# Optimization experiments

Hardware: AMD Instinct MI355X
Metric: run time of the kernel (lower is better)

The kernel has to match this reference:

```python
import jax, jax.numpy as jnp
import numpy as np

B, T, N = 16, 2048, 64
NUM_RATES, GRAPH_H, GCN_H, GATE_H, RATE_E = 8, 32, 32, 64, 16
F = T // 2 + 1


def _directional_fill(values, observed):
    # values: [B,T,N] float, observed: [B,T,N] bool. Sequential carry-forward fill.
    def step(carry, inp):
        last, has = carry
        v, obs = inp
        last = jnp.where(obs, v, last)
        has = has | obs
        filled = jnp.where(obs, v, jnp.where(has, last, jnp.zeros_like(last)))
        return (last, has), (filled, has)

    b, t, n = values.shape
    init = (jnp.zeros((b, n), values.dtype), jnp.zeros((b, n), dtype=bool))
    _, (filled, avail) = jax.lax.scan(step, init, (values.swapaxes(0, 1), observed.swapaxes(0, 1)))
    return filled.swapaxes(0, 1), avail.swapaxes(0, 1)


def warm_start_fill(values, missing_mask):
    observed = ~missing_mask.astype(bool)
    seed = jnp.where(observed, values, jnp.zeros_like(values))
    f_fill, f_av = _directional_fill(values, observed)
    b_fill, b_av = _directional_fill(values[:, ::-1], observed[:, ::-1])
    b_fill, b_av = b_fill[:, ::-1], b_av[:, ::-1]
    missing = missing_mask.astype(bool)
    both = missing & f_av & b_av
    fonly = missing & f_av & ~b_av
    bonly = missing & ~f_av & b_av
    seed = jnp.where(both, 0.5 * (f_fill + b_fill), seed)
    seed = jnp.where(fonly, f_fill, seed)
    seed = jnp.where(bonly, b_fill, seed)
    return seed


def setup_inputs() -> dict:
    key = jax.random.key(0)
    ks = jax.random.split(key, 16)
    x_input = jax.random.normal(ks[0], (B, T, N), dtype=jnp.float32)
    model_missing_mask = (jax.random.uniform(ks[1], (B, T, N)) < 0.5).astype(jnp.float32)
    rate_id = jax.random.randint(ks[2], (N,), 0, NUM_RATES)
    s = lambda k, shape, d: jax.random.normal(k, shape, dtype=jnp.float32) * (1.0 / np.sqrt(d))
    return {
        "x_input": x_input,
        "model_missing_mask": model_missing_mask,
        "rate_id": rate_id,
        "node_emb": s(ks[3], (N, GRAPH_H), GRAPH_H),
        "gcn_w1": s(ks[4], (GCN_H,), 1),
        "gcn_b1": jnp.zeros((GCN_H,), jnp.float32),
        "gcn_w2": s(ks[5], (GCN_H,), GCN_H),
        "gcn_b2": jnp.zeros((), jnp.float32),
        "freq_re": s(ks[6], (F, N), 1),
        "freq_im": s(ks[7], (F, N), 1),
        "rate_table": s(ks[8], (NUM_RATES, RATE_E), 1),
        "gw1": s(ks[9], (6 + RATE_E, GATE_H), 6 + RATE_E),
        "gb1": jnp.zeros((GATE_H,), jnp.float32),
        "gw2": s(ks[10], (GATE_H, GATE_H), GATE_H),
        "gb2": jnp.zeros((GATE_H,), jnp.float32),
        "gw3": s(ks[11], (GATE_H, 2), GATE_H),
        "gb3": jnp.zeros((2,), jnp.float32),
    }


def _forward(x_input, model_missing_mask, rate_id, node_emb, gcn_w1, gcn_b1,
             gcn_w2, gcn_b2, freq_re, freq_im, rate_table, gw1, gb1, gw2, gb2, gw3, gb3):
    x_seed = warm_start_fill(x_input, model_missing_mask)

    # --- GCN expert: learned adjacency from node embeddings, 1-hop propagation ---
    scores = jax.nn.relu(node_emb @ node_emb.T)            # [N,N]
    adjacency = jax.nn.softmax(scores, axis=-1)            # [N,N]
    h = jax.nn.gelu(x_seed[..., None] * gcn_w1 + gcn_b1)   # [B,T,N,H]
    h = jnp.einsum('nm,btmh->btnh', adjacency, h)          # message passing
    x_gcn = jnp.einsum('btnh,h->btn', h, gcn_w2) + gcn_b2  # [B,T,N]

    # --- Frequency expert: learned complex filter in rfft space ---
    X = jnp.fft.rfft(x_seed, axis=1)                       # [B,F,N]
    filt = freq_re + 1j * freq_im                          # [F,N]
    x_freq = jnp.fft.irfft(X * filt, n=T, axis=1).astype(x_seed.dtype)

    # --- Gate ---
    rate_embed = jnp.broadcast_to(rate_table[rate_id][None, None], (B, T, N, RATE_E))
    feats = jnp.stack([x_seed, model_missing_mask, x_gcn, x_freq,
                       x_gcn - x_seed, x_freq - x_seed], axis=-1)  # [B,T,N,6]
    gate_in = jnp.concatenate([feats, rate_embed], axis=-1)        # [B,T,N,22]
    g = jax.nn.gelu(gate_in @ gw1 + gb1)
    g = jax.nn.gelu(g @ gw2 + gb2)
    logits = g @ gw3 + gb3                                          # [B,T,N,2]
    logits = logits - jnp.max(logits, axis=-1, keepdims=True)
    gate_weights = jax.nn.softmax(logits, axis=-1)

    experts = jnp.stack([x_gcn, x_freq], axis=-1)                   # [B,T,N,2]
    x_imputed = jnp.sum(gate_weights * experts, axis=-1)
    x_complete = jnp.where(model_missing_mask.astype(bool), x_imputed, x_input)
    return x_seed, x_gcn, x_freq, x_imputed, x_complete, gate_weights, adjacency


def reference(x_input, model_missing_mask, rate_id, node_emb, gcn_w1, gcn_b1,
              gcn_w2, gcn_b2, freq_re, freq_im, rate_table, gw1, gb1, gw2, gb2, gw3, gb3):
    return _forward(x_input, model_missing_mask, rate_id, node_emb, gcn_w1, gcn_b1,
                    gcn_w2, gcn_b2, freq_re, freq_im, rate_table, gw1, gb1, gw2, gb2, gw3, gb3)
```

## Files before the change

### kernel.cpp

```cpp
#include <hip/hip_runtime.h>
#include <cstdint>

#define S_ELEMS 2097152ull
#define TT 2048
#define NN 64

typedef __attribute__((ext_vector_type(8))) short bf16x8;
typedef __attribute__((ext_vector_type(4))) float f32x4;

__device__ __forceinline__ float gelu_f(float x) {
  float x2 = x * x;
  float z = -1.5957691216057308f * x * (1.0f + 0.044715f * x2);
  return __fdividef(x, 1.0f + __expf(z));
}

__device__ __forceinline__ float2 cmul(float2 a, float2 b) {
  return make_float2(a.x * b.x - a.y * b.y, a.x * b.y + a.y * b.x);
}

__device__ __forceinline__ uint16_t f2bf(float x) {
  uint32_t u = __float_as_uint(x);
  return (uint16_t)((u + 0x7FFFu + ((u >> 16) & 1u)) >> 16);
}

__global__ __launch_bounds__(256) void fill_kernel(
    const float* __restrict__ x, const float* __restrict__ mask,
    float* __restrict__ seed_out, float* __restrict__ xsT)
{
  __shared__ float s_last[64][4], s_vfirst[64][4];
  __shared__ int   s_has[64][4], s_fidx[64][4];
  __shared__ float s_cl[64][4], s_bv[64][4];
  __shared__ int   s_ch[64][4], s_bh[64][4];
  __shared__ int   s_fg[4];

  const int tid = threadIdx.x;
  const int s4 = tid & 3, c = tid >> 2;
  const int b = blockIdx.x >> 4;
  const int n = ((blockIdx.x & 15) << 2) + s4;
  const size_t base = (size_t)b * (TT * NN) + n;
  const int t0 = c << 5;

  float ff[32];
  float last = 0.f; int has = 0; int fidx = TT; float vfirst = 0.f;
  #pragma unroll
  for (int i = 0; i < 32; ++i) {
    size_t off = base + (size_t)(t0 + i) * NN;
    float v = x[off];
    float m = mask[off];
    bool obs = (m == 0.0f);
    if (obs) { last = v; if (!has) { has = 1; fidx = t0 + i; vfirst = v; } }
    ff[i] = obs ? v : last;
  }
  s_last[c][s4] = last; s_has[c][s4] = has;
  s_vfirst[c][s4] = vfirst; s_fidx[c][s4] = fidx;
  __syncthreads();

  if (tid < 4) {
    float cl = 0.f; int ch = 0; int fg = TT;
    for (int cc = 0; cc < 64; ++cc) {
      s_cl[cc][tid] = cl; s_ch[cc][tid] = ch;
      if (s_has[cc][tid]) {
        cl = s_last[cc][tid]; ch = 1;
        if (fg == TT) fg = s_fidx[cc][tid];
      }
    }
    s_fg[tid] = fg;
    float bv = 0.f; int bh = 0;
    for (int cc = 63; cc >= 0; --cc) {
      s_bv[cc][tid] = bv; s_bh[cc][tid] = bh;
      if (s_has[cc][tid]) { bv = s_vfirst[cc][tid]; bh = 1; }
    }
  }
  __syncthreads();

  const float cl  = s_cl[c][s4]; const int ch  = s_ch[c][s4];
  const float bcv = s_bv[c][s4]; const int bch = s_bh[c][s4];
  const int firstg = s_fg[s4];
  const float pre = ch ? cl : 0.f;
  const int floc = fidx - t0;
  const size_t tbase = ((size_t)b * NN + n) * TT;

  float lastb = 0.f; int hasb = 0;
  float xb0, xb1, xb2, xb3;
  #pragma unroll
  for (int i = 31; i >= 0; --i) {
    int t = t0 + i;
    size_t off = base + (size_t)t * NN;
    float v = x[off];
    float m = mask[off];
    bool obs = (m == 0.0f);
    if (obs) { lastb = v; hasb = 1; }
    float bf = hasb ? lastb : bcv;
    int bav = hasb | bch;
    float ffv = (i < floc) ? pre : ff[i];
    int fav = (t >= firstg) ? 1 : 0;
    float sv;
    if (obs) sv = v;
    else if (fav && bav) sv = 0.5f * (ffv + bf);
    else if (fav) sv = ffv;
    else if (bav) sv = bf;
    else sv = 0.f;
    seed_out[off] = sv;
    if ((i & 3) == 3) xb3 = sv;
    else if ((i & 3) == 2) xb2 = sv;
    else if ((i & 3) == 1) xb1 = sv;
    else {
      xb0 = sv;
      *(float4*)(xsT + tbase + t) = make_float4(xb0, xb1, xb2, xb3);
    }
  }
}

__global__ __launch_bounds__(256) void adj_prep_kernel(
    const float* __restrict__ node_emb,
    const float* __restrict__ fre, const float* __restrict__ fim,
    float* __restrict__ adj, float2* __restrict__ filtT)
{
  const int tid = threadIdx.x;
  if (blockIdx.x == 0) {
    __shared__ float E[64 * 32];
    for (int i = tid; i < 2048; i += 256) E[i] = node_emb[i];
    __syncthreads();
    if (tid < 64) {
      float er[32];
      #pragma unroll
      for (int k = 0; k < 32; ++k) er[k] = E[tid * 32 + k];
      float sc[64];
      float mx = -1e30f;
      #pragma unroll
      for (int j = 0; j < 64; ++j) {
        float acc = 0.f;
        #pragma unroll
        for (int k = 0; k < 32; ++k) acc += er[k] * E[j * 32 + k];
        acc = fmaxf(acc, 0.f);
        sc[j] = acc;
        mx = fmaxf(mx, acc);
      }
      float sum = 0.f;
      #pragma unroll
      for (int j = 0; j < 64; ++j) { float e = __expf(sc[j] - mx); sc[j] = e; sum += e; }
      float inv = __fdividef(1.f, sum);
      #pragma unroll
      for (int j = 0; j < 64; ++j) adj[tid * 64 + j] = sc[j] * inv;
    }
  } else {
    for (int idx = (blockIdx.x - 1) * 256 + tid; idx < 1025 * 64; idx += 5 * 256) {
      int k = idx >> 6, nn = idx & 63;
      filtT[(size_t)nn * 1025 + k] = make_float2(fre[idx], fim[idx]);
    }
  }
}

__global__ __launch_bounds__(256) void gcn_kernel(
    const float* __restrict__ seed, const float* __restrict__ adj,
    const float* __restrict__ w1, const float* __restrict__ b1,
    const float* __restrict__ w2, const float* __restrict__ b2p,
    float* __restrict__ xgcn)
{
  __shared__ float At[64 * 65];
  __shared__ float su[4][64];
  __shared__ float sw1[32], sb1[32], sw2[32];
  const int tid = threadIdx.x;
  for (int i = tid; i < 4096; i += 256) {
    int nn = i >> 6, m = i & 63;
    At[m * 65 + nn] = adj[i];
  }
  if (tid < 32) { sw1[tid] = w1[tid]; sb1[tid] = b1[tid]; sw2[tid] = w2[tid]; }
  const float b2 = b2p[0];
  const int r = tid >> 6, n = tid & 63;
  const size_t row0 = (size_t)blockIdx.x * 32;

  for (int it = 0; it < 8; ++it) {
    __syncthreads();
    size_t row = row0 + it * 4 + r;
    float xv = seed[row * 64 + n];
    float u = 0.f;
    #pragma unroll
    for (int h = 0; h < 32; ++h) u += sw2[h] * gelu_f(xv * sw1[h] + sb1[h]);
    su[r][n] = u;
    __syncthreads();
    float acc = b2;
    #pragma unroll 16
    for (int m = 0; m < 64; ++m) acc += At[m * 65 + n] * su[r][m];
    xgcn[row * 64 + n] = acc;
  }
}

__global__ __launch_bounds__(256) void fft_kernel(
    const float* __restrict__ xsT, const float2* __restrict__ filtT,
    float* __restrict__ xfreq)
{
  __shared__ float2 D[2048];
  __shared__ float2 TW[1024];
  __shared__ float2 FL[1025];
  const int tid = threadIdx.x;
  const int series = blockIdx.x;
  const int bb = series >> 6, n = series & 63;

  for (int m = tid; m < 1024; m += 256) {
    float s, c;
    __sincosf(-3.0679615757712823e-3f * (float)m, &s, &c);
    TW[m] = make_float2(c, s);
  }
  {
    const float2* fsrc = filtT + (size_t)n * 1025;
    for (int i = tid; i < 1025; i += 256) FL[i] = fsrc[i];
  }
  const float* src = xsT + (size_t)series * TT;
  for (int i = tid; i < TT; i += 256) D[i] = make_float2(src[i], 0.f);
  __syncthreads();

  #pragma unroll
  for (int lh = 9; lh >= 1; lh -= 2) {
    const int h = 1 << lh;
    const int tstr = 512 >> lh;
    #pragma unroll
    for (int w = 0; w < 2; ++w) {
      const int u = tid + (w << 8);
      const int j = u & (h - 1);
      const int p = ((u >> lh) << (lh + 2)) + j;
      float2 x0 = D[p], x1 = D[p + h], x2 = D[p + 2 * h], x3 = D[p + 3 * h];
      float2 W  = TW[j * tstr];
      float2 W2 = TW[2 * j * tstr];
      float2 W3 = cmul(W, W2);
      float2 s02 = make_float2(x0.x + x2.x, x0.y + x2.y);
      float2 d02 = make_float2(x0.x - x2.x, x0.y - x2.y);
      float2 s13 = make_float2(x1.x + x3.x, x1.y + x3.y);
      float2 d13 = make_float2(x1.x - x3.x, x1.y - x3.y);
      D[p]         = make_float2(s02.x + s13.x, s02.y + s13.y);
      D[p + h]     = cmul(make_float2(s02.x - s13.x, s02.y - s13.y), W2);
      D[p + 2 * h] = cmul(make_float2(d02.x + d13.y, d02.y - d13.x), W);
      D[p + 3 * h] = cmul(make_float2(d02.x - d13.y, d02.y + d13.x), W3);
    }
    __syncthreads();
  }
  #pragma unroll
  for (int w = 0; w < 4; ++w) {
    const int u = tid + (w << 8);
    const int p = u * 2;
    float2 a = D[p], b = D[p + 1];
    D[p]     = make_float2(a.x + b.x, a.y + b.y);
    D[p + 1] = make_float2(a.x - b.x, a.y - b.y);
  }
  __syncthreads();

  for (int p = tid; p < TT; p += 256) {
    const int k = (int)(__brev((unsigned)p) >> 21);
    float2 f;
    if (k <= 1024) f = FL[k];
    else { f = FL[2048 - k]; f.y = -f.y; }
    float2 Xv = D[p];
    float pr = Xv.x * f.x - Xv.y * f.y;
    float pi = Xv.x * f.y + Xv.y * f.x;
    if (k == 0 || k == 1024) pi = 0.f;
    D[p] = make_float2(pr, pi);
  }
  __syncthreads();

  #pragma unroll
  for (int w = 0; w < 4; ++w) {
    const int u = tid + (w << 8);
    const int p = u * 2;
    float2 a = D[p], b = D[p + 1];
    D[p]     = make_float2(a.x + b.x, a.y + b.y);
    D[p + 1] = make_float2(a.x - b.x, a.y - b.y);
  }
  __syncthreads();
  #pragma unroll
  for (int lh = 1; lh <= 9; lh += 2) {
    const int h = 1 << lh;
    const int tstr = 512 >> lh;
    #pragma unroll
    for (int w = 0; w < 2; ++w) {
      const int u = tid + (w << 8);
      const int j = u & (h - 1);
      const int p = ((u >> lh) << (lh + 2)) + j;
      float2 z0 = D[p], z1 = D[p + h], z2 = D[p + 2 * h], z3 = D[p + 3 * h];
      float2 W  = TW[j * tstr];
      float2 W2 = TW[2 * j * tstr];
      float2 cW  = make_float2(W.x, -W.y);
      float2 cW2 = make_float2(W2.x, -W2.y);
      float2 icW = make_float2(-cW.y, cW.x);
      float2 t1 = cmul(z1, cW2);
      float2 y0 = make_float2(z0.x + t1.x, z0.y + t1.y);
      float2 y1 = make_float2(z0.x - t1.x, z0.y - t1.y);
      float2 t3 = cmul(z3, cW2);
      float2 y2 = make_float2(z2.x + t3.x, z2.y + t3.y);
      float2 y3 = make_float2(z2.x - t3.x, z2.y - t3.y);
      float2 u2 = cmul(y2, cW);
      float2 u3 = cmul(y3, icW);
      D[p]         = make_float2(y0.x + u2.x, y0.y + u2.y);
      D[p + 2 * h] = make_float2(y0.x - u2.x, y0.y - u2.y);
      D[p + h]     = make_float2(y1.x + u3.x, y1.y + u3.y);
      D[p + 3 * h] = make_float2(y1.x - u3.x, y1.y - u3.y);
    }
    __syncthreads();
  }

  const float inv = (1.0f / 2048.0f);
  const size_t obase = (size_t)bb * (TT * NN) + n;
  for (int t2 = tid; t2 < TT; t2 += 256) {
    xfreq[obase + (size_t)t2 * NN] = D[t2].x * inv;
  }
}

__global__ __launch_bounds__(256) void mlp_kernel(
    const float* __restrict__ xin, const float* __restrict__ mask, const int* __restrict__ rate_id,
    const float* __restrict__ rate_table,
    const float* __restrict__ gw1, const float* __restrict__ gb1,
    const float* __restrict__ gw2, const float* __restrict__ gb2,
    const float* __restrict__ gw3, const float* __restrict__ gb3,
    float* __restrict__ out)
{
  __shared__ uint16_t A_lds[128 * 72];
  __shared__ uint16_t Wt_lds[64 * 72];
  __shared__ __align__(16) float s_l1[512];
  __shared__ float s_b1rT[512];
  __shared__ float s_w3d[64], s_gb2[64];
  __shared__ float s_seed[128], s_gcn[128], s_freq[128], s_mask[128], s_xin[128];
  __shared__ float s_d[128];
  __shared__ int s_rid[64];
  const int tid = threadIdx.x;
  const size_t blk_base = (size_t)blockIdx.x * 128;

  for (int i = tid; i < 4096; i += 256) {
    int h = i >> 6, k = i & 63;
    Wt_lds[h * 72 + k] = f2bf(gw2[k * 64 + h]);
  }
  for (int i = tid; i < 512; i += 256) {
    int k = i >> 3, c = i & 7;
    s_l1[i] = (c < 6) ? gw1[c * 64 + k] : 0.f;
  }
  for (int i = tid; i < 512; i += 256) {
    int k = i >> 3, r = i & 7;
    float acc = gb1[k];
    #pragma unroll
    for (int e = 0; e < 16; ++e) acc += rate_table[r * 16 + e] * gw1[(6 + e) * 64 + k];
    s_b1rT[i] = acc;
  }
  if (tid < 64) {
    s_w3d[tid] = gw3[tid * 2] - gw3[tid * 2 + 1];
    s_gb2[tid] = gb2[tid];
    s_rid[tid] = rate_id[tid];
  }
  if (tid < 128) {
    size_t g = blk_base + tid;
    s_seed[tid] = out[g];
    s_gcn[tid]  = out[S_ELEMS + g];
    s_freq[tid] = out[2 * S_ELEMS + g];
  } else {
    int e = tid - 128;
    size_t g = blk_base + e;
    s_mask[e] = mask[g];
    s_xin[e]  = xin[g];
  }
  __syncthreads();

  {
    const int e = tid & 127, half = tid >> 7;
    const float f0 = s_seed[e], f1 = s_mask[e], f2 = s_gcn[e], f3 = s_freq[e];
    const float f4 = f2 - f0, f5 = f3 - f0;
    const int rid = s_rid[e & 63];
    const float4* l1v = (const float4*)s_l1;
    #pragma unroll
    for (int i = 0; i < 16; ++i) {
      const int k0 = half * 32 + 2 * i;
      float4 wA0 = l1v[k0 * 2],       wB0 = l1v[k0 * 2 + 1];
      float4 wA1 = l1v[k0 * 2 + 2],   wB1 = l1v[k0 * 2 + 3];
      float a0 = s_b1rT[k0 * 8 + rid]
               + wA0.x * f0 + wA0.y * f1 + wA0.z * f2 + wA0.w * f3 + wB0.x * f4 + wB0.y * f5;
      float a1 = s_b1rT[(k0 + 1) * 8 + rid]
               + wA1.x * f0 + wA1.y * f1 + wA1.z * f2 + wA1.w * f3 + wB1.x * f4 + wB1.y * f5;
      uint32_t pk = (uint32_t)f2bf(gelu_f(a0)) | ((uint32_t)f2bf(gelu_f(a1)) << 16);
      *(uint32_t*)&A_lds[e * 72 + k0] = pk;
    }
  }
  __syncthreads();

  const int lane = tid & 63, wv = tid >> 6;
  const int r16 = lane & 15, g4 = lane >> 4;
  {
    const uint16_t* Ar0 = &A_lds[(wv * 32 +      r16) * 72 + g4 * 8];
    const uint16_t* Ar1 = &A_lds[(wv * 32 + 16 + r16) * 72 + g4 * 8];
    const uint16_t* Wr  = &Wt_lds[r16 * 72 + g4 * 8];

    f32x4 acc00 = {0.f,0.f,0.f,0.f}, acc01 = {0.f,0.f,0.f,0.f};
    f32x4 acc02 = {0.f,0.f,0.f,0.f}, acc03 = {0.f,0.f,0.f,0.f};
    f32x4 acc10 = {0.f,0.f,0.f,0.f}, acc11 = {0.f,0.f,0.f,0.f};
    f32x4 acc12 = {0.f,0.f,0.f,0.f}, acc13 = {0.f,0.f,0.f,0.f};

    #pragma unroll
    for (int kk = 0; kk < 2; ++kk) {
      const int ko = kk * 32;
      bf16x8 a0 = *(const bf16x8*)(Ar0 + ko);
      bf16x8 a1 = *(const bf16x8*)(Ar1 + ko);
      bf16x8 b0 = *(const bf16x8*)(Wr + ko);
      bf16x8 b1 = *(const bf16x8*)(Wr + 16 * 72 + ko);
      bf16x8 b2 = *(const bf16x8*)(Wr + 32 * 72 + ko);
      bf16x8 b3 = *(const bf16x8*)(Wr + 48 * 72 + ko);
      acc00 = __builtin_amdgcn_mfma_f32_16x16x32_bf16(a0, b0, acc00, 0, 0, 0);
      acc01 = __builtin_amdgcn_mfma_f32_16x16x32_bf16(a0, b1, acc01, 0, 0, 0);
      acc02 = __builtin_amdgcn_mfma_f32_16x16x32_bf16(a0, b2, acc02, 0, 0, 0);
      acc03 = __builtin_amdgcn_mfma_f32_16x16x32_bf16(a0, b3, acc03, 0, 0, 0);
      acc10 = __builtin_amdgcn_mfma_f32_16x16x32_bf16(a1, b0, acc10, 0, 0, 0);
      acc11 = __builtin_amdgcn_mfma_f32_16x16x32_bf16(a1, b1, acc11, 0, 0, 0);
      acc12 = __builtin_amdgcn_mfma_f32_16x16x32_bf16(a1, b2, acc12, 0, 0, 0);
      acc13 = __builtin_amdgcn_mfma_f32_16x16x32_bf16(a1, b3, acc13, 0, 0, 0);
    }

    const float gA = s_gb2[r16],      gB = s_gb2[16 + r16];
    const float gC = s_gb2[32 + r16], gD = s_gb2[48 + r16];
    const float wA = s_w3d[r16],      wB = s_w3d[16 + r16];
    const float wC = s_w3d[32 + r16], wD = s_w3d[48 + r16];

#define ROWRED(tr, v, A0, A1, A2, A3) { \
    float p = gelu_f(A0[v] + gA) * wA + gelu_f(A1[v] + gB) * wB \
            + gelu_f(A2[v] + gC) * wC + gelu_f(A3[v] + gD) * wD; \
    p += __shfl_xor(p, 1, 64); p += __shfl_xor(p, 2, 64); \
    p += __shfl_xor(p, 4, 64); p += __shfl_xor(p, 8, 64); \
    if (r16 == 0) s_d[wv * 32 + tr * 16 + g4 * 4 + v] = p; }

    ROWRED(0, 0, acc00, acc01, acc02, acc03)
    ROWRED(0, 1, acc00, acc01, acc02, acc03)
    ROWRED(0, 2, acc00, acc01, acc02, acc03)
    ROWRED(0, 3, acc00, acc01, acc02, acc03)
    ROWRED(1, 0, acc10, acc11, acc12, acc13)
    ROWRED(1, 1, acc10, acc11, acc12, acc13)
    ROWRED(1, 2, acc10, acc11, acc12, acc13)
    ROWRED(1, 3, acc10, acc11, acc12, acc13)
#undef ROWRED
  }
  __syncthreads();

  if (tid < 128) {
    const size_t g = blk_base + tid;
    float d = s_d[tid] + gb3[0] - gb3[1];
    float w0 = __fdividef(1.0f, 1.0f + __expf(-d));
    float w1g = 1.0f - w0;
    float ximp = w0 * s_gcn[tid] + w1g * s_freq[tid];
    out[3 * S_ELEMS + g] = ximp;
    out[4 * S_ELEMS + g] = (s_mask[tid] != 0.0f) ? ximp : s_xin[tid];
    ((float2*)(out + 5 * S_ELEMS))[g] = make_float2(w0, w1g);
  }
}

extern "C" void kernel_launch(void* const* d_in, const int* in_sizes, int n_in,
                              void* d_out, int out_size, void* d_ws, size_t ws_size,
                              hipStream_t stream) {
  (void)in_sizes; (void)n_in; (void)out_size; (void)d_ws; (void)ws_size;
  const float* x_input    = (const float*)d_in[0];
  const float* mask       = (const float*)d_in[1];
  const int*   rate_id    = (const int*)d_in[2];
  const float* node_emb   = (const float*)d_in[3];
  const float* gcn_w1     = (const float*)d_in[4];
  const float* gcn_b1     = (const float*)d_in[5];
  const float* gcn_w2     = (const float*)d_in[6];
  const float* gcn_b2     = (const float*)d_in[7];
  const float* freq_re    = (const float*)d_in[8];
  const float* freq_im    = (const float*)d_in[9];
  const float* rate_table = (const float*)d_in[10];
  const float* gw1        = (const float*)d_in[11];
  const float* gb1        = (const float*)d_in[12];
  const float* gw2        = (const float*)d_in[13];
  const float* gb2        = (const float*)d_in[14];
  const float* gw3        = (const float*)d_in[15];
  const float* gb3        = (const float*)d_in[16];
  float* out = (float*)d_out;

  float* out0 = out;
  float* out1 = out + S_ELEMS;
  float* out2 = out + 2 * S_ELEMS;
  float* out4 = out + 4 * S_ELEMS;
  float* out6 = out + 7 * S_ELEMS;
  float2* filtT = (float2*)(out + 5 * S_ELEMS);

  fill_kernel<<<256, 256, 0, stream>>>(x_input, mask, out0, out4);
  adj_prep_kernel<<<6, 256, 0, stream>>>(node_emb, freq_re, freq_im, out6, filtT);
  gcn_kernel<<<1024, 256, 0, stream>>>(out0, out6, gcn_w1, gcn_b1, gcn_w2, gcn_b2, out1);
  fft_kernel<<<1024, 256, 0, stream>>>(out4, filtT, out2);
  mlp_kernel<<<16384, 256, 0, stream>>>(x_input, mask, rate_id, rate_table,
                                        gw1, gb1, gw2, gb2, gw3, gb3, out);
}
```

Baseline: 500.6 us.

## Make MLP kernel persistent over 8 chunks and compute layer-1 directly into MFMA fragments

The MLP kernel now processes 8 chunks of 128 elements per block, cutting the grid from 16384 to 2048 blocks so the per-block weight staging (gw2 transpose to bf16, folded rate-bias table) is amortized. Layer-1 activations are computed in registers directly in the MFMA A-operand layout instead of being written to and reread from an LDS tile, which removes A_lds and one barrier. The bias table is padded to stride 9, the gw2 load is made coalesced, and launch bounds request 3 blocks per CU. The tradeoffs are redundant layer-1 compute across lanes (each lane recomputes 8 k-values per row) and fewer blocks to hide latency.

```diff
diff --git a/kernel.cpp b/kernel.cpp
--- a/kernel.cpp
+++ b/kernel.cpp
@@ -304,7 +304,7 @@
   }
 }
 
-__global__ __launch_bounds__(256) void mlp_kernel(
+__global__ __launch_bounds__(256, 3) void mlp_kernel(
     const float* __restrict__ xin, const float* __restrict__ mask, const int* __restrict__ rate_id,
     const float* __restrict__ rate_table,
     const float* __restrict__ gw1, const float* __restrict__ gb1,
@@ -312,20 +312,18 @@
     const float* __restrict__ gw3, const float* __restrict__ gb3,
     float* __restrict__ out)
 {
-  __shared__ uint16_t A_lds[128 * 72];
   __shared__ uint16_t Wt_lds[64 * 72];
   __shared__ __align__(16) float s_l1[512];
-  __shared__ float s_b1rT[512];
+  __shared__ float s_b1rT[64 * 9];
   __shared__ float s_w3d[64], s_gb2[64];
-  __shared__ float s_seed[128], s_gcn[128], s_freq[128], s_mask[128], s_xin[128];
+  __shared__ float s_feat[5][128];
   __shared__ float s_d[128];
   __shared__ int s_rid[64];
   const int tid = threadIdx.x;
-  const size_t blk_base = (size_t)blockIdx.x * 128;
 
   for (int i = tid; i < 4096; i += 256) {
-    int h = i >> 6, k = i & 63;
-    Wt_lds[h * 72 + k] = f2bf(gw2[k * 64 + h]);
+    int k = i >> 6, h = i & 63;
+    Wt_lds[h * 72 + k] = f2bf(gw2[i]);
   }
   for (int i = tid; i < 512; i += 256) {
     int k = i >> 3, c = i & 7;
@@ -336,53 +334,44 @@
     float acc = gb1[k];
     #pragma unroll
     for (int e = 0; e < 16; ++e) acc += rate_table[r * 16 + e] * gw1[(6 + e) * 64 + k];
-    s_b1rT[i] = acc;
+    s_b1rT[k * 9 + r] = acc;
   }
   if (tid < 64) {
     s_w3d[tid] = gw3[tid * 2] - gw3[tid * 2 + 1];
     s_gb2[tid] = gb2[tid];
     s_rid[tid] = rate_id[tid];
   }
-  if (tid < 128) {
-    size_t g = blk_base + tid;
-    s_seed[tid] = out[g];
-    s_gcn[tid]  = out[S_ELEMS + g];
-    s_freq[tid] = out[2 * S_ELEMS + g];
-  } else {
-    int e = tid - 128;
-    size_t g = blk_base + e;
-    s_mask[e] = mask[g];
-    s_xin[e]  = xin[g];
-  }
-  __syncthreads();
-
-  {
-    const int e = tid & 127, half = tid >> 7;
-    const float f0 = s_seed[e], f1 = s_mask[e], f2 = s_gcn[e], f3 = s_freq[e];
-    const float f4 = f2 - f0, f5 = f3 - f0;
-    const int rid = s_rid[e & 63];
-    const float4* l1v = (const float4*)s_l1;
-    #pragma unroll
-    for (int i = 0; i < 16; ++i) {
-      const int k0 = half * 32 + 2 * i;
-      float4 wA0 = l1v[k0 * 2],       wB0 = l1v[k0 * 2 + 1];
-      float4 wA1 = l1v[k0 * 2 + 2],   wB1 = l1v[k0 * 2 + 3];
-      float a0 = s_b1rT[k0 * 8 + rid]
-               + wA0.x * f0 + wA0.y * f1 + wA0.z * f2 + wA0.w * f3 + wB0.x * f4 + wB0.y * f5;
-      float a1 = s_b1rT[(k0 + 1) * 8 + rid]
-               + wA1.x * f0 + wA1.y * f1 + wA1.z * f2 + wA1.w * f3 + wB1.x * f4 + wB1.y * f5;
-      uint32_t pk = (uint32_t)f2bf(gelu_f(a0)) | ((uint32_t)f2bf(gelu_f(a1)) << 16);
-      *(uint32_t*)&A_lds[e * 72 + k0] = pk;
-    }
-  }
-  __syncthreads();
+  const float dbias = gb3[0] - gb3[1];
 
   const int lane = tid & 63, wv = tid >> 6;
   const int r16 = lane & 15, g4 = lane >> 4;
-  {
-    const uint16_t* Ar0 = &A_lds[(wv * 32 +      r16) * 72 + g4 * 8];
-    const uint16_t* Ar1 = &A_lds[(wv * 32 + 16 + r16) * 72 + g4 * 8];
-    const uint16_t* Wr  = &Wt_lds[r16 * 72 + g4 * 8];
+  const float4* l1v = (const float4*)s_l1;
+
+  for (int ch = 0; ch < 8; ++ch) {
+    const size_t blk_base = ((size_t)blockIdx.x * 8 + ch) * 128;
+    __syncthreads();
+    if (tid < 128) {
+      size_t g = blk_base + tid;
+      s_feat[0][tid] = out[g];
+      s_feat[1][tid] = out[S_ELEMS + g];
+      s_feat[2][tid] = out[2 * S_ELEMS + g];
+    } else {
+      int e = tid - 128;
+      size_t g = blk_base + e;
+      s_feat[3][e] = mask[g];
+      s_feat[4][e] = xin[g];
+    }
+    __syncthreads();
+
+    const int e0 = wv * 32 + r16, e1 = e0 + 16;
+    const float s0 = s_feat[0][e0], m0 = s_feat[3][e0];
+    const float g0 = s_feat[1][e0], q0 = s_feat[2][e0];
+    const float s1 = s_feat[0][e1], m1 = s_feat[3][e1];
+    const float g1 = s_feat[1][e1], q1 = s_feat[2][e1];
+    const float d0 = g0 - s0, p0 = q0 - s0;
+    const float d1 = g1 - s1, p1 = q1 - s1;
+    const int rid0 = s_rid[e0 & 63];
+    const int rid1 = s_rid[e1 & 63];
 
     f32x4 acc00 = {0.f,0.f,0.f,0.f}, acc01 = {0.f,0.f,0.f,0.f};
     f32x4 acc02 = {0.f,0.f,0.f,0.f}, acc03 = {0.f,0.f,0.f,0.f};
@@ -390,14 +379,24 @@
     f32x4 acc12 = {0.f,0.f,0.f,0.f}, acc13 = {0.f,0.f,0.f,0.f};
 
     #pragma unroll
-    for (int kk = 0; kk < 2; ++kk) {
-      const int ko = kk * 32;
-      bf16x8 a0 = *(const bf16x8*)(Ar0 + ko);
-      bf16x8 a1 = *(const bf16x8*)(Ar1 + ko);
-      bf16x8 b0 = *(const bf16x8*)(Wr + ko);
-      bf16x8 b1 = *(const bf16x8*)(Wr + 16 * 72 + ko);
-      bf16x8 b2 = *(const bf16x8*)(Wr + 32 * 72 + ko);
-      bf16x8 b3 = *(const bf16x8*)(Wr + 48 * 72 + ko);
+    for (int ks = 0; ks < 2; ++ks) {
+      bf16x8 a0, a1;
+      #pragma unroll
+      for (int j = 0; j < 8; ++j) {
+        const int k = ks * 32 + g4 * 8 + j;
+        float4 wA = l1v[k * 2], wB = l1v[k * 2 + 1];
+        float bb0 = s_b1rT[k * 9 + rid0];
+        float bb1 = s_b1rT[k * 9 + rid1];
+        float v0 = bb0 + wA.x * s0 + wA.y * m0 + wA.z * g0 + wA.w * q0 + wB.x * d0 + wB.y * p0;
+        float v1 = bb1 + wA.x * s1 + wA.y * m1 + wA.z * g1 + wA.w * q1 + wB.x * d1 + wB.y * p1;
+        a0[j] = (short)f2bf(gelu_f(v0));
+        a1[j] = (short)f2bf(gelu_f(v1));
+      }
+      const uint16_t* Wr = &Wt_lds[r16 * 72 + ks * 32 + g4 * 8];
+      bf16x8 b0 = *(const bf16x8*)(Wr);
+      bf16x8 b1 = *(const bf16x8*)(Wr + 16 * 72);
+      bf16x8 b2 = *(const bf16x8*)(Wr + 32 * 72);
+      bf16x8 b3 = *(const bf16x8*)(Wr + 48 * 72);
       acc00 = __builtin_amdgcn_mfma_f32_16x16x32_bf16(a0, b0, acc00, 0, 0, 0);
       acc01 = __builtin_amdgcn_mfma_f32_16x16x32_bf16(a0, b1, acc01, 0, 0, 0);
       acc02 = __builtin_amdgcn_mfma_f32_16x16x32_bf16(a0, b2, acc02, 0, 0, 0);
@@ -408,39 +407,41 @@
       acc13 = __builtin_amdgcn_mfma_f32_16x16x32_bf16(a1, b3, acc13, 0, 0, 0);
     }
 
-    const float gA = s_gb2[r16],      gB = s_gb2[16 + r16];
-    const float gC = s_gb2[32 + r16], gD = s_gb2[48 + r16];
-    const float wA = s_w3d[r16],      wB = s_w3d[16 + r16];
-    const float wC = s_w3d[32 + r16], wD = s_w3d[48 + r16];
+    {
+      const float gA = s_gb2[r16],      gB = s_gb2[16 + r16];
+      const float gC = s_gb2[32 + r16], gD = s_gb2[48 + r16];
+      const float wA = s_w3d[r16],      wB = s_w3d[16 + r16];
+      const float wC = s_w3d[32 + r16], wD = s_w3d[48 + r16];
 
 #define ROWRED(tr, v, A0, A1, A2, A3) { \
-    float p = gelu_f(A0[v] + gA) * wA + gelu_f(A1[v] + gB) * wB \
-            + gelu_f(A2[v] + gC) * wC + gelu_f(A3[v] + gD) * wD; \
-    p += __shfl_xor(p, 1, 64); p += __shfl_xor(p, 2, 64); \
-    p += __shfl_xor(p, 4, 64); p += __shfl_xor(p, 8, 64); \
-    if (r16 == 0) s_d[wv * 32 + tr * 16 + g4 * 4 + v] = p; }
-
-    ROWRED(0, 0, acc00, acc01, acc02, acc03)
-    ROWRED(0, 1, acc00, acc01, acc02, acc03)
-    ROWRED(0, 2, acc00, acc01, acc02, acc03)
-    ROWRED(0, 3, acc00, acc01, acc02, acc03)
-    ROWRED(1, 0, acc10, acc11, acc12, acc13)
-    ROWRED(1, 1, acc10, acc11, acc12, acc13)
-    ROWRED(1, 2, acc10, acc11, acc12, acc13)
-    ROWRED(1, 3, acc10, acc11, acc12, acc13)
+      float p = gelu_f(A0[v] + gA) * wA + gelu_f(A1[v] + gB) * wB \
+              + gelu_f(A2[v] + gC) * wC + gelu_f(A3[v] + gD) * wD; \
+      p += __shfl_xor(p, 1, 64); p += __shfl_xor(p, 2, 64); \
+      p += __shfl_xor(p, 4, 64); p += __shfl_xor(p, 8, 64); \
+      if (r16 == 0) s_d[wv * 32 + tr * 16 + g4 * 4 + v] = p; }
+
+      ROWRED(0, 0, acc00, acc01, acc02, acc03)
+      ROWRED(0, 1, acc00, acc01, acc02, acc03)
+      ROWRED(0, 2, acc00, acc01, acc02, acc03)
+      ROWRED(0, 3, acc00, acc01, acc02, acc03)
+      ROWRED(1, 0, acc10, acc11, acc12, acc13)
+      ROWRED(1, 1, acc10, acc11, acc12, acc13)
+      ROWRED(1, 2, acc10, acc11, acc12, acc13)
+      ROWRED(1, 3, acc10, acc11, acc12, acc13)
 #undef ROWRED
-  }
-  __syncthreads();
-
-  if (tid < 128) {
-    const size_t g = blk_base + tid;
-    float d = s_d[tid] + gb3[0] - gb3[1];
-    float w0 = __fdividef(1.0f, 1.0f + __expf(-d));
-    float w1g = 1.0f - w0;
-    float ximp = w0 * s_gcn[tid] + w1g * s_freq[tid];
-    out[3 * S_ELEMS + g] = ximp;
-    out[4 * S_ELEMS + g] = (s_mask[tid] != 0.0f) ? ximp : s_xin[tid];
-    ((float2*)(out + 5 * S_ELEMS))[g] = make_float2(w0, w1g);
+    }
+    __syncthreads();
+
+    if (tid < 128) {
+      const size_t g = blk_base + tid;
+      float d = s_d[tid] + dbias;
+      float w0 = __fdividef(1.0f, 1.0f + __expf(-d));
+      float w1g = 1.0f - w0;
+      float ximp = w0 * s_feat[1][tid] + w1g * s_feat[2][tid];
+      out[3 * S_ELEMS + g] = ximp;
+      out[4 * S_ELEMS + g] = (s_feat[3][tid] != 0.0f) ? ximp : s_feat[4][tid];
+      ((float2*)(out + 5 * S_ELEMS))[g] = make_float2(w0, w1g);
+    }
   }
 }
 
@@ -478,6 +479,6 @@
   adj_prep_kernel<<<6, 256, 0, stream>>>(node_emb, freq_re, freq_im, out6, filtT);
   gcn_kernel<<<1024, 256, 0, stream>>>(out0, out6, gcn_w1, gcn_b1, gcn_w2, gcn_b2, out1);
   fft_kernel<<<1024, 256, 0, stream>>>(out4, filtT, out2);
-  mlp_kernel<<<16384, 256, 0, stream>>>(x_input, mask, rate_id, rate_table,
-                                        gw1, gb1, gw2, gb2, gw3, gb3, out);
-}
+  mlp_kernel<<<2048, 256, 0, stream>>>(x_input, mask, rate_id, rate_table,
+                                       gw1, gb1, gw2, gb2, gw3, gb3, out);
+}
```

Result: faster. 470.4 us (-6.0%).
